# Performance work log

Measured on AMD Instinct MI355X. Metric: run time of the kernel, lower is better.

## Reference

```python
import jax, jax.numpy as jnp
import numpy as np
from jax import lax

GN_EPS = 1e-5


def _conv2d(x, w, b, pad):
    # x: (N, C, H, W), w: (O, I, kh, kw)
    y = lax.conv_general_dilated(x, w, window_strides=(1, 1),
                                 padding=[(pad, pad), (pad, pad)],
                                 dimension_numbers=('NCHW', 'OIHW', 'NCHW'))
    return y + b[None, :, None, None]


def _eca(x, eca_w, eca_b):
    # x: (N, C, H, W) -> channel attention (N, C, 1, 1)
    y = jnp.mean(x, axis=(2, 3))[:, None, :]  # (N, 1, C) : GAP then treat C as length
    y = lax.conv_general_dilated(y, eca_w, window_strides=(1,),
                                 padding=[(1, 1)],
                                 dimension_numbers=('NCH', 'OIH', 'NCH'))
    y = jax.nn.sigmoid(y + eca_b[None, :, None])  # (N, 1, C)
    return y[:, 0, :, None, None]  # (N, C, 1, 1)


def _group_norm_per_channel(x, gn_w, gn_b):
    # num_groups == num_channels: normalize each channel over (H, W)
    mean = jnp.mean(x, axis=(2, 3), keepdims=True)
    var = jnp.var(x, axis=(2, 3), keepdims=True)
    xhat = (x - mean) * lax.rsqrt(var + GN_EPS)
    return xhat * gn_w[None, :, None, None] + gn_b[None, :, None, None]


def setup_inputs() -> dict:
    key = jax.random.key(0)
    ks = jax.random.split(key, 8)
    b, c, h, w = 16, 512, 64, 64
    cg = c // 32  # 16
    s = 1.0 / np.sqrt(cg)
    return {
        'x': jax.random.normal(ks[0], (b, c, h, w), jnp.float32),
        'conv1x1_w': jax.random.normal(ks[1], (cg, cg, 1, 1), jnp.float32) * s,
        'conv1x1_b': jnp.zeros((cg,), jnp.float32),
        'conv3x3_w': jax.random.normal(ks[2], (cg, cg, 3, 3), jnp.float32) * (s / 3),
        'conv3x3_b': jnp.zeros((cg,), jnp.float32),
        'conv5x5_w': jax.random.normal(ks[3], (cg, cg, 5, 5), jnp.float32) * (s / 5),
        'conv5x5_b': jnp.zeros((cg,), jnp.float32),
        'gn_w': jnp.ones((cg,), jnp.float32),
        'gn_b': jnp.zeros((cg,), jnp.float32),
        'eca_w': jax.random.normal(ks[4], (1, 1, 3), jnp.float32) * 0.5,
        'eca_b': jnp.zeros((1,), jnp.float32),
        'groups': 32,
    }


def reference(x, conv1x1_w, conv1x1_b, conv3x3_w, conv3x3_b,
              conv5x5_w, conv5x5_b, gn_w, gn_b, eca_w, eca_b, groups):
    b, c, h, w = x.shape
    cg = c // groups
    bg = b * groups
    group_x = x.reshape(bg, cg, h, w)

    # coordinate attention branch
    x_h = jnp.mean(group_x, axis=3, keepdims=True)            # (bg, cg, h, 1)
    x_w = jnp.mean(group_x, axis=2, keepdims=True)            # (bg, cg, 1, w)
    x_w_t = jnp.transpose(x_w, (0, 1, 3, 2))                  # (bg, cg, w, 1)
    hw = _conv2d(jnp.concatenate([x_h, x_w_t], axis=2), conv1x1_w, conv1x1_b, 0)
    x_h2, x_w2 = hw[:, :, :h, :], hw[:, :, h:, :]             # (bg,cg,h,1), (bg,cg,w,1)
    gated = group_x * jax.nn.sigmoid(x_h2) * jax.nn.sigmoid(jnp.transpose(x_w2, (0, 1, 3, 2)))
    x1 = _group_norm_per_channel(gated, gn_w, gn_b)

    # parallel conv branches
    x2 = _conv2d(group_x, conv3x3_w, conv3x3_b, 1)
    x3 = _conv2d(group_x, conv5x5_w, conv5x5_b, 2)

    # shared ECA channel attention over the three branches
    ca = _eca(x1, eca_w, eca_b) + _eca(x2, eca_w, eca_b) + _eca(x3, eca_w, eca_b)
    group_x = group_x * ca

    # cross-scale softmax-bmm interactions
    def chan_softmax(v):
        # (bg, cg, h, w) -> softmax over channel means -> (bg, 1, cg)
        return jax.nn.softmax(jnp.mean(v, axis=(2, 3)), axis=-1)[:, None, :]

    x11, x21, x31 = chan_softmax(x1), chan_softmax(x2), chan_softmax(x3)
    f1 = x1.reshape(bg, cg, h * w)
    f2 = x2.reshape(bg, cg, h * w)
    f3 = x3.reshape(bg, cg, h * w)

    weights = (jnp.matmul(x11, f2) + jnp.matmul(x11, f3)
               + jnp.matmul(x21, f1) + jnp.matmul(x21, f3)
               + jnp.matmul(x31, f1) + jnp.matmul(x31, f2))  # (bg, 1, h*w)
    weights = jax.nn.sigmoid(weights.reshape(bg, 1, h, w))

    return (group_x * weights).reshape(b, c, h, w)
```

## Files before the change

kernel.cpp:

```cpp
#include <hip/hip_runtime.h>

typedef unsigned int u32;

#define CG   16
#define HWN  4096
#define LSTR 72

__device__ __forceinline__ float sigm(float x) { return 1.0f / (1.0f + __expf(-x)); }

union SharedU {
  struct {
    float row[16][64];
    float col[16][64];
    union {
      float cwave[16][4][64];
      struct { float RS[16][25]; float part2[16][16]; float part3[16][16]; } r;
    } u;
  } p;
  float cb[2][68][LSTR];
};

__global__ __launch_bounds__(256, 2) void ema_kernel(
    const float* __restrict__ x,
    const float* __restrict__ w1, const float* __restrict__ b1,
    const float* __restrict__ w3, const float* __restrict__ b3,
    const float* __restrict__ w5, const float* __restrict__ b5,
    const float* __restrict__ gnw, const float* __restrict__ gnb,
    const float* __restrict__ ew, const float* __restrict__ eb,
    float* __restrict__ out)
{
  __shared__ SharedU U;
  __shared__ float s_sh[16][64];
  __shared__ float s_sw[16][64];
  __shared__ float s_W5[16][28];
  __shared__ float s_ca[16], s_A1[16], s_Cc[16];
  __shared__ float s_w1[256], s_b1[16], s_gnw[16], s_gnb[16], s_b3[16], s_b5[16], s_ecaw[3], s_ecab[1];
  __shared__ float s_m2[16], s_m3[16], s_sm1[16], s_sm2[16], s_sm3[16];
  __shared__ float s_a1[16], s_a2[16], s_a3[16], s_total[16];
  __shared__ float s_red[16][4][2];
  __shared__ float s_scal[2];

  const int g = blockIdx.x;
  const int t = threadIdx.x;
  const float* px   = x   + (size_t)g * CG * HWN;
  float*       pout = out + (size_t)g * CG * HWN;

  {
    const int j4 = t & 15, hh = t >> 4, wv4 = t >> 6;
    for (int c = 0; c < CG; ++c) {
      float cp0 = 0.f, cp1 = 0.f, cp2 = 0.f, cp3 = 0.f;
      #pragma unroll
      for (int k = 0; k < 4; ++k) {
        int y = 4 * hh + k;
        float4 v = *(const float4*)(px + c * HWN + y * 64 + 4 * j4);
        float rs = v.x + v.y + v.z + v.w;
        rs += __shfl_xor(rs, 1); rs += __shfl_xor(rs, 2);
        rs += __shfl_xor(rs, 4); rs += __shfl_xor(rs, 8);
        if (j4 == 0) U.p.row[c][y] = rs;
        cp0 += v.x; cp1 += v.y; cp2 += v.z; cp3 += v.w;
      }
      cp0 += __shfl_xor(cp0, 16); cp0 += __shfl_xor(cp0, 32);
      cp1 += __shfl_xor(cp1, 16); cp1 += __shfl_xor(cp1, 32);
      cp2 += __shfl_xor(cp2, 16); cp2 += __shfl_xor(cp2, 32);
      cp3 += __shfl_xor(cp3, 16); cp3 += __shfl_xor(cp3, 32);
      if ((t & 48) == 0) *(float4*)&U.p.u.cwave[c][wv4][4 * j4] = make_float4(cp0, cp1, cp2, cp3);
    }
  }
  s_w1[t] = w1[t];
  if (t < 16) {
    s_b1[t]  = b1[t];  s_gnw[t] = gnw[t]; s_gnb[t] = gnb[t];
    s_b3[t]  = b3[t];  s_b5[t]  = b5[t];
  }
  if (t < 3)  s_ecaw[t] = ew[t];
  if (t == 0) s_ecab[0] = eb[0];
  __syncthreads();

  {
    int c = t >> 4, q = t & 15;
    float4 s = make_float4(0.f, 0.f, 0.f, 0.f);
    #pragma unroll
    for (int w = 0; w < 4; ++w) {
      float4 v = *(float4*)&U.p.u.cwave[c][w][4 * q];
      s.x += v.x; s.y += v.y; s.z += v.z; s.w += v.w;
    }
    *(float4*)&U.p.col[c][4 * q] = s;
  }
  __syncthreads();
  if (t < 16) { float s = 0.f; for (int y = 0; y < 64; ++y) s += U.p.row[t][y]; s_total[t] = s; }
  __syncthreads();

  for (int m = 0; m < 8; ++m) {
    int idx = t + 256 * m; int o = idx >> 7, pos = idx & 127;
    float acc = s_b1[o];
    const float inv64 = 1.0f / 64.0f;
    #pragma unroll
    for (int i = 0; i < 16; ++i) {
      float v = (pos < 64 ? U.p.row[i][pos] : U.p.col[i][pos - 64]) * inv64;
      acc += s_w1[o * 16 + i] * v;
    }
    float sg = sigm(acc);
    if (pos < 64) s_sh[o][pos] = sg; else s_sw[o][pos - 64] = sg;
  }
  for (int m = 0; m < 2; ++m) {
    int task = t + 256 * m;
    if (task < 400) {
      int i = task / 25, kk = task % 25;
      int dy = kk / 5 - 2, dx = kk % 5 - 2;
      int a  = dy > 0 ? dy : 0,   b  = 64 + (dy < 0 ? dy : 0);
      int cl = dx > 0 ? dx : 0,   d  = 64 + (dx < 0 ? dx : 0);
      float S = s_total[i];
      if (a > 0)  S -= U.p.row[i][0];
      if (a > 1)  S -= U.p.row[i][1];
      if (b < 64) S -= U.p.row[i][63];
      if (b < 63) S -= U.p.row[i][62];
      for (int x0 = 0; x0 < cl; ++x0) {
        float cv = U.p.col[i][x0];
        if (a > 0)  cv -= px[i * HWN + 0 * 64  + x0];
        if (a > 1)  cv -= px[i * HWN + 1 * 64  + x0];
        if (b < 64) cv -= px[i * HWN + 63 * 64 + x0];
        if (b < 63) cv -= px[i * HWN + 62 * 64 + x0];
        S -= cv;
      }
      for (int x0 = d; x0 < 64; ++x0) {
        float cv = U.p.col[i][x0];
        if (a > 0)  cv -= px[i * HWN + 0 * 64  + x0];
        if (a > 1)  cv -= px[i * HWN + 1 * 64  + x0];
        if (b < 64) cv -= px[i * HWN + 63 * 64 + x0];
        if (b < 63) cv -= px[i * HWN + 62 * 64 + x0];
        S -= cv;
      }
      U.p.u.r.RS[i][kk] = S;
    }
  }
  __syncthreads();

  {
    int o = t >> 4, i = t & 15;
    float p2 = 0.f, p3 = 0.f;
    const float* w3b = w3 + (o * 16 + i) * 9;
    const float* w5b = w5 + (o * 16 + i) * 25;
    #pragma unroll
    for (int ky = 0; ky < 3; ++ky)
      #pragma unroll
      for (int kx = 0; kx < 3; ++kx)
        p2 += w3b[ky * 3 + kx] * U.p.u.r.RS[i][(ky + 1) * 5 + (kx + 1)];
    #pragma unroll
    for (int kk = 0; kk < 25; ++kk) p3 += w5b[kk] * U.p.u.r.RS[i][kk];
    U.p.u.r.part2[o][i] = p2; U.p.u.r.part3[o][i] = p3;
  }
  __syncthreads();
  if (t < 16)      { float s = 0.f; for (int i = 0; i < 16; ++i) s += U.p.u.r.part2[t][i];    s_m2[t] = s_b3[t] + s * (1.0f/4096.0f); }
  else if (t < 32) { int o = t - 16; float s = 0.f; for (int i = 0; i < 16; ++i) s += U.p.u.r.part3[o][i]; s_m3[o] = s_b5[o] + s * (1.0f/4096.0f); }
  __syncthreads();

  if (t < 3) {
    const float* m = (t == 0) ? s_gnb : (t == 1) ? s_m2 : s_m3;
    float* dst     = (t == 0) ? s_sm1 : (t == 1) ? s_sm2 : s_sm3;
    float mx = m[0];
    for (int c = 1; c < 16; ++c) mx = fmaxf(mx, m[c]);
    float e[16], ssum = 0.f;
    for (int c = 0; c < 16; ++c) { e[c] = __expf(m[c] - mx); ssum += e[c]; }
    float r = 1.0f / ssum;
    for (int c = 0; c < 16; ++c) dst[c] = e[c] * r;
  }
  __syncthreads();

  if (t < 16) {
    int c = t;
    float casum = 0.f;
    #pragma unroll
    for (int v = 0; v < 3; ++v) {
      const float* m = (v == 0) ? s_gnb : (v == 1) ? s_m2 : s_m3;
      float acc = s_ecab[0] + s_ecaw[1] * m[c];
      if (c > 0)  acc += s_ecaw[0] * m[c - 1];
      if (c < 15) acc += s_ecaw[2] * m[c + 1];
      casum += sigm(acc);
    }
    s_ca[c] = casum;
    s_a1[c] = s_sm2[c] + s_sm3[c];
    s_a2[c] = s_sm1[c] + s_sm3[c];
    s_a3[c] = s_sm1[c] + s_sm2[c];
  }
  __syncthreads();

  if (t == 0) {
    float s = 0.f;
    for (int o = 0; o < 16; ++o) s += s_a2[o] * s_b3[o] + s_a3[o] * s_b5[o];
    s_scal[1] = s;
  }
  for (int m = 0; m < 2; ++m) {
    int task = t + 256 * m;
    if (task < 400) {
      int i = task / 25, kk = task % 25, ky = kk / 5, kx = kk % 5;
      float acc = 0.f;
      #pragma unroll
      for (int o = 0; o < 16; ++o) acc += s_a3[o] * w5[((o * 16 + i) * 5 + ky) * 5 + kx];
      if (ky >= 1 && ky <= 3 && kx >= 1 && kx <= 3) {
        #pragma unroll
        for (int o = 0; o < 16; ++o) acc += s_a2[o] * w3[((o * 16 + i) * 3 + (ky - 1)) * 3 + (kx - 1)];
      }
      s_W5[i][kk] = acc;
    }
    else if (task < 448) { int i = (task - 400) / 3; s_W5[i][25 + (task - 400) % 3] = 0.f; }
  }
  __syncthreads();

  for (int m = 0; m < 10; ++m) { int idx = t + 256 * m; if (idx < 2448) ((float4*)U.cb)[idx] = make_float4(0.f, 0.f, 0.f, 0.f); }
  __syncthreads();

  const int x0 = 4 * (t & 15), y0 = 4 * (t >> 4), wv4 = t >> 6;

  #define STAGE(buf, c) {                                              \
    _Pragma("unroll")                                                  \
    for (int k = 0; k < 4; ++k) {                                      \
      int q = t + 256 * k;                                             \
      int rr = q >> 4, xc = (q & 15) * 4;                              \
      float4 v = *(const float4*)(px + (c) * HWN + rr * 64 + xc);      \
      float* d = &U.cb[buf][2 + rr][2 + xc];                           \
      *(float2*)d       = make_float2(v.x, v.y);                       \
      *(float2*)(d + 2) = make_float2(v.z, v.w);                       \
    }                                                                  \
  }

  float ws[16];
  #pragma unroll
  for (int i = 0; i < 16; ++i) ws[i] = 0.f;

  STAGE(0, 0);
  __syncthreads();
  #pragma unroll 1
  for (int c = 0; c < 16; ++c) {
    if (c < 15) STAGE((c + 1) & 1, c + 1);
    float Wk[28];
    #pragma unroll
    for (int i = 0; i < 7; ++i) *(float4*)&Wk[4 * i] = *(float4*)&s_W5[c][4 * i];
    float shv[4], swv[4];
    #pragma unroll
    for (int r = 0; r < 4; ++r) { shv[r] = s_sh[c][y0 + r]; swv[r] = s_sw[c][x0 + r]; }
    const float* base = &U.cb[c & 1][0][0];
    float gsl = 0.f, gql = 0.f;
    #pragma unroll
    for (int q = 0; q < 8; ++q) {
      const float* rp = base + (y0 + q) * LSTR + x0;
      float4 A = *(const float4*)rp, B = *(const float4*)(rp + 4);
      float v[8] = {A.x, A.y, A.z, A.w, B.x, B.y, B.z, B.w};
      if (q >= 2 && q <= 5) {
        const int ry = q - 2;
        #pragma unroll
        for (int m = 0; m < 4; ++m) { float gg = v[m + 2] * shv[ry] * swv[m]; gsl += gg; gql += gg * gg; }
      }
      #pragma unroll
      for (int r = 0; r < 4; ++r) {
        if (q - r >= 0 && q - r <= 4) {
          const int kr = q - r;
          #pragma unroll
          for (int m = 0; m < 4; ++m) {
            float a = ws[4 * r + m];
            a += Wk[kr * 5 + 0] * v[m + 0];
            a += Wk[kr * 5 + 1] * v[m + 1];
            a += Wk[kr * 5 + 2] * v[m + 2];
            a += Wk[kr * 5 + 3] * v[m + 3];
            a += Wk[kr * 5 + 4] * v[m + 4];
            ws[4 * r + m] = a;
          }
        }
      }
    }
    gsl += __shfl_xor(gsl, 1);  gql += __shfl_xor(gql, 1);
    gsl += __shfl_xor(gsl, 2);  gql += __shfl_xor(gql, 2);
    gsl += __shfl_xor(gsl, 4);  gql += __shfl_xor(gql, 4);
    gsl += __shfl_xor(gsl, 8);  gql += __shfl_xor(gql, 8);
    gsl += __shfl_xor(gsl, 16); gql += __shfl_xor(gql, 16);
    gsl += __shfl_xor(gsl, 32); gql += __shfl_xor(gql, 32);
    if ((t & 63) == 0) { s_red[c][wv4][0] = gsl; s_red[c][wv4][1] = gql; }
    __syncthreads();
  }

  if (t < 16) {
    int c = t;
    float S = 0.f, Q = 0.f;
    #pragma unroll
    for (int w = 0; w < 4; ++w) { S += s_red[c][w][0]; Q += s_red[c][w][1]; }
    float mu  = S * (1.0f / 4096.0f);
    float var = Q * (1.0f / 4096.0f) - mu * mu;
    float inv = rsqrtf(var + 1e-5f);
    s_A1[c] = s_a1[c] * s_gnw[c] * inv;
    s_Cc[c] = s_a1[c] * (s_gnb[c] - mu * s_gnw[c] * inv);
  }
  __syncthreads();
  if (t == 0) { float s = s_scal[1]; for (int c = 0; c < 16; ++c) s += s_Cc[c]; s_scal[0] = s; }
  for (int m = 0; m < 4; ++m) { int idx = t + 256 * m; int c = idx >> 6, y = idx & 63; s_sh[c][y] *= s_A1[c]; }
  __syncthreads();

  float gws[16];
  #pragma unroll
  for (int i = 0; i < 16; ++i) gws[i] = 0.f;
  #pragma unroll 1
  for (int c = 0; c < 16; ++c) {
    float shv[4], swv[4];
    #pragma unroll
    for (int r = 0; r < 4; ++r) { shv[r] = s_sh[c][y0 + r]; swv[r] = s_sw[c][x0 + r]; }
    #pragma unroll
    for (int r = 0; r < 4; ++r) {
      float4 xv = *(const float4*)(px + c * HWN + (y0 + r) * 64 + x0);
      gws[4 * r + 0] += shv[r] * swv[0] * xv.x;
      gws[4 * r + 1] += shv[r] * swv[1] * xv.y;
      gws[4 * r + 2] += shv[r] * swv[2] * xv.z;
      gws[4 * r + 3] += shv[r] * swv[3] * xv.w;
    }
  }
  {
    const float Cc = s_scal[0];
    #pragma unroll
    for (int i = 0; i < 16; ++i) ws[i] = sigm(ws[i] + gws[i] + Cc);
  }
  #pragma unroll 1
  for (int c = 0; c < 16; ++c) {
    float cav = s_ca[c];
    #pragma unroll
    for (int r = 0; r < 4; ++r) {
      float4 xv = *(const float4*)(px + c * HWN + (y0 + r) * 64 + x0);
      float4 o;
      o.x = xv.x * cav * ws[4 * r + 0];
      o.y = xv.y * cav * ws[4 * r + 1];
      o.z = xv.z * cav * ws[4 * r + 2];
      o.w = xv.w * cav * ws[4 * r + 3];
      *(float4*)(pout + c * HWN + (y0 + r) * 64 + x0) = o;
    }
  }
}

extern "C" void kernel_launch(void* const* d_in, const int* in_sizes, int n_in,
                              void* d_out, int out_size, void* d_ws, size_t ws_size,
                              hipStream_t stream) {
  const float* X  = (const float*)d_in[0];
  const float* W1 = (const float*)d_in[1];
  const float* B1 = (const float*)d_in[2];
  const float* W3 = (const float*)d_in[3];
  const float* B3 = (const float*)d_in[4];
  const float* W5 = (const float*)d_in[5];
  const float* B5 = (const float*)d_in[6];
  const float* GW = (const float*)d_in[7];
  const float* GB = (const float*)d_in[8];
  const float* EW = (const float*)d_in[9];
  const float* EB = (const float*)d_in[10];
  float* O = (float*)d_out;
  ema_kernel<<<dim3(512), dim3(256), 0, stream>>>(X, W1, B1, W3, B3, W5, B5, GW, GB, EW, EB, O);
}
```

Before: 345.5 us.

## Double block size, fuse GN-gate pass into conv loop with deferred per-channel scaling

Launches 512 threads per group block, so each thread handles a 2x4 output tile instead of 4x4. The first-pass reductions are restructured so each wave owns two channels, which removes the cross-wave column reduction and one barrier. The separate pass that re-read x for the gated GroupNorm contribution is removed. Instead, gated values are kept in registers and folded into the accumulator with a two-channel lag once each channel's GN statistics are ready. The shared-memory union is dropped in favour of separate arrays with a tighter LDS stride, which raises LDS use and register pressure in exchange for fewer global re-reads and barriers.

```diff
diff --git a/kernel.cpp b/kernel.cpp
--- a/kernel.cpp
+++ b/kernel.cpp
@@ -4,23 +4,11 @@
 
 #define CG   16
 #define HWN  4096
-#define LSTR 72
+#define LSTR 68
 
 __device__ __forceinline__ float sigm(float x) { return 1.0f / (1.0f + __expf(-x)); }
 
-union SharedU {
-  struct {
-    float row[16][64];
-    float col[16][64];
-    union {
-      float cwave[16][4][64];
-      struct { float RS[16][25]; float part2[16][16]; float part3[16][16]; } r;
-    } u;
-  } p;
-  float cb[2][68][LSTR];
-};
-
-__global__ __launch_bounds__(256, 2) void ema_kernel(
+__global__ __launch_bounds__(512, 4) void ema_kernel(
     const float* __restrict__ x,
     const float* __restrict__ w1, const float* __restrict__ b1,
     const float* __restrict__ w3, const float* __restrict__ b3,
@@ -29,44 +17,57 @@
     const float* __restrict__ ew, const float* __restrict__ eb,
     float* __restrict__ out)
 {
-  __shared__ SharedU U;
-  __shared__ float s_sh[16][64];
-  __shared__ float s_sw[16][64];
-  __shared__ float s_W5[16][28];
+  __shared__ __align__(16) float s_cb[2][68][LSTR];
+  __shared__ __align__(16) float s_row[16][64];
+  __shared__ __align__(16) float s_col[16][64];
+  __shared__ __align__(16) float s_RS[16][25];
+  __shared__ float s_p2[16][16], s_p3[16][16];
+  __shared__ __align__(16) float s_sh[16][64];
+  __shared__ __align__(16) float s_sw[16][64];
+  __shared__ __align__(16) float s_W5[16][28];
   __shared__ float s_ca[16], s_A1[16], s_Cc[16];
   __shared__ float s_w1[256], s_b1[16], s_gnw[16], s_gnb[16], s_b3[16], s_b5[16], s_ecaw[3], s_ecab[1];
   __shared__ float s_m2[16], s_m3[16], s_sm1[16], s_sm2[16], s_sm3[16];
   __shared__ float s_a1[16], s_a2[16], s_a3[16], s_total[16];
-  __shared__ float s_red[16][4][2];
+  __shared__ float s_red[16][8][2];
   __shared__ float s_scal[2];
 
   const int g = blockIdx.x;
   const int t = threadIdx.x;
+  const int wv = t >> 6;
+  const int ln = t & 63;
   const float* px   = x   + (size_t)g * CG * HWN;
   float*       pout = out + (size_t)g * CG * HWN;
 
   {
-    const int j4 = t & 15, hh = t >> 4, wv4 = t >> 6;
-    for (int c = 0; c < CG; ++c) {
+    const int j4 = ln & 15;
+    const int rr = ln >> 4;
+    #pragma unroll 1
+    for (int cc = 0; cc < 2; ++cc) {
+      const int c = 2 * wv + cc;
+      float rs[16];
       float cp0 = 0.f, cp1 = 0.f, cp2 = 0.f, cp3 = 0.f;
       #pragma unroll
-      for (int k = 0; k < 4; ++k) {
-        int y = 4 * hh + k;
-        float4 v = *(const float4*)(px + c * HWN + y * 64 + 4 * j4);
-        float rs = v.x + v.y + v.z + v.w;
-        rs += __shfl_xor(rs, 1); rs += __shfl_xor(rs, 2);
-        rs += __shfl_xor(rs, 4); rs += __shfl_xor(rs, 8);
-        if (j4 == 0) U.p.row[c][y] = rs;
+      for (int j = 0; j < 16; ++j) {
+        float4 v = *(const float4*)(px + c * HWN + (rr + 4 * j) * 64 + 4 * j4);
+        rs[j] = v.x + v.y + v.z + v.w;
         cp0 += v.x; cp1 += v.y; cp2 += v.z; cp3 += v.w;
+      }
+      #pragma unroll
+      for (int j = 0; j < 16; ++j) {
+        float r = rs[j];
+        r += __shfl_xor(r, 1); r += __shfl_xor(r, 2);
+        r += __shfl_xor(r, 4); r += __shfl_xor(r, 8);
+        if (j4 == 0) s_row[c][rr + 4 * j] = r;
       }
       cp0 += __shfl_xor(cp0, 16); cp0 += __shfl_xor(cp0, 32);
       cp1 += __shfl_xor(cp1, 16); cp1 += __shfl_xor(cp1, 32);
       cp2 += __shfl_xor(cp2, 16); cp2 += __shfl_xor(cp2, 32);
       cp3 += __shfl_xor(cp3, 16); cp3 += __shfl_xor(cp3, 32);
-      if ((t & 48) == 0) *(float4*)&U.p.u.cwave[c][wv4][4 * j4] = make_float4(cp0, cp1, cp2, cp3);
-    }
-  }
-  s_w1[t] = w1[t];
+      if (rr == 0) *(float4*)&s_col[c][4 * j4] = make_float4(cp0, cp1, cp2, cp3);
+    }
+  }
+  if (t < 256) s_w1[t] = w1[t];
   if (t < 16) {
     s_b1[t]  = b1[t];  s_gnw[t] = gnw[t]; s_gnb[t] = gnb[t];
     s_b3[t]  = b3[t];  s_b5[t]  = b5[t];
@@ -75,66 +76,55 @@
   if (t == 0) s_ecab[0] = eb[0];
   __syncthreads();
 
-  {
-    int c = t >> 4, q = t & 15;
-    float4 s = make_float4(0.f, 0.f, 0.f, 0.f);
-    #pragma unroll
-    for (int w = 0; w < 4; ++w) {
-      float4 v = *(float4*)&U.p.u.cwave[c][w][4 * q];
-      s.x += v.x; s.y += v.y; s.z += v.z; s.w += v.w;
-    }
-    *(float4*)&U.p.col[c][4 * q] = s;
-  }
-  __syncthreads();
-  if (t < 16) { float s = 0.f; for (int y = 0; y < 64; ++y) s += U.p.row[t][y]; s_total[t] = s; }
-  __syncthreads();
-
-  for (int m = 0; m < 8; ++m) {
-    int idx = t + 256 * m; int o = idx >> 7, pos = idx & 127;
+  if (t < 16) { float s = 0.f; for (int y = 0; y < 64; ++y) s += s_row[t][y]; s_total[t] = s; }
+  __syncthreads();
+
+  #pragma unroll
+  for (int m = 0; m < 4; ++m) {
+    int idx = t + 512 * m; int o = idx >> 7, pos = idx & 127;
     float acc = s_b1[o];
     const float inv64 = 1.0f / 64.0f;
     #pragma unroll
     for (int i = 0; i < 16; ++i) {
-      float v = (pos < 64 ? U.p.row[i][pos] : U.p.col[i][pos - 64]) * inv64;
+      float v = (pos < 64 ? s_row[i][pos] : s_col[i][pos - 64]) * inv64;
       acc += s_w1[o * 16 + i] * v;
     }
     float sg = sigm(acc);
     if (pos < 64) s_sh[o][pos] = sg; else s_sw[o][pos - 64] = sg;
   }
-  for (int m = 0; m < 2; ++m) {
-    int task = t + 256 * m;
-    if (task < 400) {
-      int i = task / 25, kk = task % 25;
-      int dy = kk / 5 - 2, dx = kk % 5 - 2;
-      int a  = dy > 0 ? dy : 0,   b  = 64 + (dy < 0 ? dy : 0);
-      int cl = dx > 0 ? dx : 0,   d  = 64 + (dx < 0 ? dx : 0);
-      float S = s_total[i];
-      if (a > 0)  S -= U.p.row[i][0];
-      if (a > 1)  S -= U.p.row[i][1];
-      if (b < 64) S -= U.p.row[i][63];
-      if (b < 63) S -= U.p.row[i][62];
-      for (int x0 = 0; x0 < cl; ++x0) {
-        float cv = U.p.col[i][x0];
-        if (a > 0)  cv -= px[i * HWN + 0 * 64  + x0];
-        if (a > 1)  cv -= px[i * HWN + 1 * 64  + x0];
-        if (b < 64) cv -= px[i * HWN + 63 * 64 + x0];
-        if (b < 63) cv -= px[i * HWN + 62 * 64 + x0];
-        S -= cv;
-      }
-      for (int x0 = d; x0 < 64; ++x0) {
-        float cv = U.p.col[i][x0];
-        if (a > 0)  cv -= px[i * HWN + 0 * 64  + x0];
-        if (a > 1)  cv -= px[i * HWN + 1 * 64  + x0];
-        if (b < 64) cv -= px[i * HWN + 63 * 64 + x0];
-        if (b < 63) cv -= px[i * HWN + 62 * 64 + x0];
-        S -= cv;
-      }
-      U.p.u.r.RS[i][kk] = S;
-    }
-  }
-  __syncthreads();
-
-  {
+  #pragma unroll
+  for (int m = 0; m < 5; ++m) { int idx = t + 512 * m; if (idx < 2312) ((float4*)s_cb)[idx] = make_float4(0.f, 0.f, 0.f, 0.f); }
+  if (t < 400) {
+    int i = t / 25, kk = t % 25;
+    int dy = kk / 5 - 2, dx = kk % 5 - 2;
+    int a  = dy > 0 ? dy : 0,   b  = 64 + (dy < 0 ? dy : 0);
+    int cl = dx > 0 ? dx : 0,   d  = 64 + (dx < 0 ? dx : 0);
+    float S = s_total[i];
+    if (a > 0)  S -= s_row[i][0];
+    if (a > 1)  S -= s_row[i][1];
+    if (b < 64) S -= s_row[i][63];
+    if (b < 63) S -= s_row[i][62];
+    for (int x0 = 0; x0 < cl; ++x0) {
+      float cv = s_col[i][x0];
+      if (a > 0)  cv -= px[i * HWN + 0 * 64  + x0];
+      if (a > 1)  cv -= px[i * HWN + 1 * 64  + x0];
+      if (b < 64) cv -= px[i * HWN + 63 * 64 + x0];
+      if (b < 63) cv -= px[i * HWN + 62 * 64 + x0];
+      S -= cv;
+    }
+    for (int x0 = d; x0 < 64; ++x0) {
+      float cv = s_col[i][x0];
+      if (a > 0)  cv -= px[i * HWN + 0 * 64  + x0];
+      if (a > 1)  cv -= px[i * HWN + 1 * 64  + x0];
+      if (b < 64) cv -= px[i * HWN + 63 * 64 + x0];
+      if (b < 63) cv -= px[i * HWN + 62 * 64 + x0];
+      S -= cv;
+    }
+    s_RS[i][kk] = S;
+  }
+  __syncthreads();
+
+  if (t < 256) {
     int o = t >> 4, i = t & 15;
     float p2 = 0.f, p3 = 0.f;
     const float* w3b = w3 + (o * 16 + i) * 9;
@@ -143,14 +133,14 @@
     for (int ky = 0; ky < 3; ++ky)
       #pragma unroll
       for (int kx = 0; kx < 3; ++kx)
-        p2 += w3b[ky * 3 + kx] * U.p.u.r.RS[i][(ky + 1) * 5 + (kx + 1)];
-    #pragma unroll
-    for (int kk = 0; kk < 25; ++kk) p3 += w5b[kk] * U.p.u.r.RS[i][kk];
-    U.p.u.r.part2[o][i] = p2; U.p.u.r.part3[o][i] = p3;
-  }
-  __syncthreads();
-  if (t < 16)      { float s = 0.f; for (int i = 0; i < 16; ++i) s += U.p.u.r.part2[t][i];    s_m2[t] = s_b3[t] + s * (1.0f/4096.0f); }
-  else if (t < 32) { int o = t - 16; float s = 0.f; for (int i = 0; i < 16; ++i) s += U.p.u.r.part3[o][i]; s_m3[o] = s_b5[o] + s * (1.0f/4096.0f); }
+        p2 += w3b[ky * 3 + kx] * s_RS[i][(ky + 1) * 5 + (kx + 1)];
+    #pragma unroll
+    for (int kk = 0; kk < 25; ++kk) p3 += w5b[kk] * s_RS[i][kk];
+    s_p2[o][i] = p2; s_p3[o][i] = p3;
+  }
+  __syncthreads();
+  if (t < 16)      { float s = 0.f; for (int i = 0; i < 16; ++i) s += s_p2[t][i];      s_m2[t] = s_b3[t] + s * (1.0f/4096.0f); }
+  else if (t < 32) { int o = t - 16; float s = 0.f; for (int i = 0; i < 16; ++i) s += s_p3[o][i]; s_m3[o] = s_b5[o] + s * (1.0f/4096.0f); }
   __syncthreads();
 
   if (t < 3) {
@@ -183,15 +173,26 @@
   }
   __syncthreads();
 
+  #define STAGE(buf, c) {                                                \
+    _Pragma("unroll")                                                    \
+    for (int k = 0; k < 2; ++k) {                                        \
+      int q = t + 512 * k;                                               \
+      int rr = q >> 4, xc = (q & 15) * 4;                                \
+      float4 v = *(const float4*)(px + (size_t)(c) * HWN + rr * 64 + xc);\
+      float* d = &s_cb[buf][2 + rr][2 + xc];                             \
+      *(float2*)d       = make_float2(v.x, v.y);                         \
+      *(float2*)(d + 2) = make_float2(v.z, v.w);                         \
+    }                                                                    \
+  }
+
   if (t == 0) {
     float s = 0.f;
     for (int o = 0; o < 16; ++o) s += s_a2[o] * s_b3[o] + s_a3[o] * s_b5[o];
     s_scal[1] = s;
   }
-  for (int m = 0; m < 2; ++m) {
-    int task = t + 256 * m;
-    if (task < 400) {
-      int i = task / 25, kk = task % 25, ky = kk / 5, kx = kk % 5;
+  if (t < 448) {
+    if (t < 400) {
+      int i = t / 25, kk = t % 25, ky = kk / 5, kx = kk % 5;
       float acc = 0.f;
       #pragma unroll
       for (int o = 0; o < 16; ++o) acc += s_a3[o] * w5[((o * 16 + i) * 5 + ky) * 5 + kx];
@@ -200,59 +201,67 @@
         for (int o = 0; o < 16; ++o) acc += s_a2[o] * w3[((o * 16 + i) * 3 + (ky - 1)) * 3 + (kx - 1)];
       }
       s_W5[i][kk] = acc;
-    }
-    else if (task < 448) { int i = (task - 400) / 3; s_W5[i][25 + (task - 400) % 3] = 0.f; }
-  }
-  __syncthreads();
-
-  for (int m = 0; m < 10; ++m) { int idx = t + 256 * m; if (idx < 2448) ((float4*)U.cb)[idx] = make_float4(0.f, 0.f, 0.f, 0.f); }
-  __syncthreads();
-
-  const int x0 = 4 * (t & 15), y0 = 4 * (t >> 4), wv4 = t >> 6;
-
-  #define STAGE(buf, c) {                                              \
-    _Pragma("unroll")                                                  \
-    for (int k = 0; k < 4; ++k) {                                      \
-      int q = t + 256 * k;                                             \
-      int rr = q >> 4, xc = (q & 15) * 4;                              \
-      float4 v = *(const float4*)(px + (c) * HWN + rr * 64 + xc);      \
-      float* d = &U.cb[buf][2 + rr][2 + xc];                           \
-      *(float2*)d       = make_float2(v.x, v.y);                       \
-      *(float2*)(d + 2) = make_float2(v.z, v.w);                       \
-    }                                                                  \
-  }
-
-  float ws[16];
+    } else {
+      int q = t - 400; s_W5[q / 3][25 + q % 3] = 0.f;
+    }
+  }
+  STAGE(0, 0);
+  __syncthreads();
+
+  const int x0 = 4 * (t & 15);
+  const int y0 = 2 * (t >> 4);
+
+  float ws[8];
   #pragma unroll
-  for (int i = 0; i < 16; ++i) ws[i] = 0.f;
-
-  STAGE(0, 0);
-  __syncthreads();
+  for (int i = 0; i < 8; ++i) ws[i] = 0.f;
+  float gsv[2][8];
+
   #pragma unroll 1
   for (int c = 0; c < 16; ++c) {
     if (c < 15) STAGE((c + 1) & 1, c + 1);
+    if (c >= 1 && t == 0) {
+      float S = 0.f, Q = 0.f;
+      #pragma unroll
+      for (int w = 0; w < 8; ++w) { S += s_red[c-1][w][0]; Q += s_red[c-1][w][1]; }
+      float mu  = S * (1.0f / 4096.0f);
+      float var = Q * (1.0f / 4096.0f) - mu * mu;
+      float inv = rsqrtf(var + 1e-5f);
+      s_A1[c-1] = s_a1[c-1] * s_gnw[c-1] * inv;
+      s_Cc[c-1] = s_a1[c-1] * (s_gnb[c-1] - mu * s_gnw[c-1] * inv);
+    }
+    if (c >= 2) {
+      float a1v = s_A1[c-2];
+      #pragma unroll
+      for (int i = 0; i < 8; ++i) ws[i] += a1v * gsv[c & 1][i];
+    }
     float Wk[28];
     #pragma unroll
     for (int i = 0; i < 7; ++i) *(float4*)&Wk[4 * i] = *(float4*)&s_W5[c][4 * i];
-    float shv[4], swv[4];
-    #pragma unroll
-    for (int r = 0; r < 4; ++r) { shv[r] = s_sh[c][y0 + r]; swv[r] = s_sw[c][x0 + r]; }
-    const float* base = &U.cb[c & 1][0][0];
+    float shv0 = s_sh[c][y0], shv1 = s_sh[c][y0 + 1];
+    float swv[4];
+    #pragma unroll
+    for (int r = 0; r < 4; ++r) swv[r] = s_sw[c][x0 + r];
+    const float* base = &s_cb[c & 1][0][0] + y0 * LSTR + x0;
     float gsl = 0.f, gql = 0.f;
     #pragma unroll
-    for (int q = 0; q < 8; ++q) {
-      const float* rp = base + (y0 + q) * LSTR + x0;
+    for (int q = 0; q < 6; ++q) {
+      const float* rp = base + q * LSTR;
       float4 A = *(const float4*)rp, B = *(const float4*)(rp + 4);
       float v[8] = {A.x, A.y, A.z, A.w, B.x, B.y, B.z, B.w};
-      if (q >= 2 && q <= 5) {
-        const int ry = q - 2;
+      if (q == 2 || q == 3) {
+        const float sh_ = (q == 2) ? shv0 : shv1;
+        const int ri = q - 2;
         #pragma unroll
-        for (int m = 0; m < 4; ++m) { float gg = v[m + 2] * shv[ry] * swv[m]; gsl += gg; gql += gg * gg; }
-      }
-      #pragma unroll
-      for (int r = 0; r < 4; ++r) {
-        if (q - r >= 0 && q - r <= 4) {
-          const int kr = q - r;
+        for (int m = 0; m < 4; ++m) {
+          float gg = v[m + 2] * sh_ * swv[m];
+          gsl += gg; gql += gg * gg;
+          gsv[c & 1][4 * ri + m] = gg;
+        }
+      }
+      #pragma unroll
+      for (int r = 0; r < 2; ++r) {
+        const int kr = q - r;
+        if (kr >= 0 && kr <= 4) {
           #pragma unroll
           for (int m = 0; m < 4; ++m) {
             float a = ws[4 * r + m];
@@ -272,61 +281,45 @@
     gsl += __shfl_xor(gsl, 8);  gql += __shfl_xor(gql, 8);
     gsl += __shfl_xor(gsl, 16); gql += __shfl_xor(gql, 16);
     gsl += __shfl_xor(gsl, 32); gql += __shfl_xor(gql, 32);
-    if ((t & 63) == 0) { s_red[c][wv4][0] = gsl; s_red[c][wv4][1] = gql; }
+    if (ln == 0) { s_red[c][wv][0] = gsl; s_red[c][wv][1] = gql; }
     __syncthreads();
   }
 
-  if (t < 16) {
-    int c = t;
+  if (t == 0) {
     float S = 0.f, Q = 0.f;
     #pragma unroll
-    for (int w = 0; w < 4; ++w) { S += s_red[c][w][0]; Q += s_red[c][w][1]; }
+    for (int w = 0; w < 8; ++w) { S += s_red[15][w][0]; Q += s_red[15][w][1]; }
     float mu  = S * (1.0f / 4096.0f);
     float var = Q * (1.0f / 4096.0f) - mu * mu;
     float inv = rsqrtf(var + 1e-5f);
-    s_A1[c] = s_a1[c] * s_gnw[c] * inv;
-    s_Cc[c] = s_a1[c] * (s_gnb[c] - mu * s_gnw[c] * inv);
-  }
-  __syncthreads();
-  if (t == 0) { float s = s_scal[1]; for (int c = 0; c < 16; ++c) s += s_Cc[c]; s_scal[0] = s; }
-  for (int m = 0; m < 4; ++m) { int idx = t + 256 * m; int c = idx >> 6, y = idx & 63; s_sh[c][y] *= s_A1[c]; }
-  __syncthreads();
-
-  float gws[16];
+    s_A1[15] = s_a1[15] * s_gnw[15] * inv;
+    s_Cc[15] = s_a1[15] * (s_gnb[15] - mu * s_gnw[15] * inv);
+    float s = s_scal[1];
+    for (int c = 0; c < 16; ++c) s += s_Cc[c];
+    s_scal[0] = s;
+  }
+  __syncthreads();
+  {
+    const float a14 = s_A1[14], a15 = s_A1[15], Ct = s_scal[0];
+    #pragma unroll
+    for (int i = 0; i < 8; ++i)
+      ws[i] = sigm(ws[i] + a14 * gsv[0][i] + a15 * gsv[1][i] + Ct);
+  }
+
   #pragma unroll
-  for (int i = 0; i < 16; ++i) gws[i] = 0.f;
-  #pragma unroll 1
   for (int c = 0; c < 16; ++c) {
-    float shv[4], swv[4];
-    #pragma unroll
-    for (int r = 0; r < 4; ++r) { shv[r] = s_sh[c][y0 + r]; swv[r] = s_sw[c][x0 + r]; }
-    #pragma unroll
-    for (int r = 0; r < 4; ++r) {
-      float4 xv = *(const float4*)(px + c * HWN + (y0 + r) * 64 + x0);
-      gws[4 * r + 0] += shv[r] * swv[0] * xv.x;
-      gws[4 * r + 1] += shv[r] * swv[1] * xv.y;
-      gws[4 * r + 2] += shv[r] * swv[2] * xv.z;
-      gws[4 * r + 3] += shv[r] * swv[3] * xv.w;
-    }
-  }
-  {
-    const float Cc = s_scal[0];
-    #pragma unroll
-    for (int i = 0; i < 16; ++i) ws[i] = sigm(ws[i] + gws[i] + Cc);
-  }
-  #pragma unroll 1
-  for (int c = 0; c < 16; ++c) {
-    float cav = s_ca[c];
-    #pragma unroll
-    for (int r = 0; r < 4; ++r) {
-      float4 xv = *(const float4*)(px + c * HWN + (y0 + r) * 64 + x0);
-      float4 o;
-      o.x = xv.x * cav * ws[4 * r + 0];
-      o.y = xv.y * cav * ws[4 * r + 1];
-      o.z = xv.z * cav * ws[4 * r + 2];
-      o.w = xv.w * cav * ws[4 * r + 3];
-      *(float4*)(pout + c * HWN + (y0 + r) * 64 + x0) = o;
-    }
+    const float cav = s_ca[c];
+    const float* xp = px   + c * HWN + y0 * 64 + x0;
+    float*       op = pout + c * HWN + y0 * 64 + x0;
+    float4 xa = *(const float4*)xp;
+    float4 xb = *(const float4*)(xp + 64);
+    float4 oa, ob;
+    oa.x = xa.x * cav * ws[0]; oa.y = xa.y * cav * ws[1];
+    oa.z = xa.z * cav * ws[2]; oa.w = xa.w * cav * ws[3];
+    ob.x = xb.x * cav * ws[4]; ob.y = xb.y * cav * ws[5];
+    ob.z = xb.z * cav * ws[6]; ob.w = xb.w * cav * ws[7];
+    *(float4*)op        = oa;
+    *(float4*)(op + 64) = ob;
   }
 }
 
@@ -345,5 +338,5 @@
   const float* EW = (const float*)d_in[9];
   const float* EB = (const float*)d_in[10];
   float* O = (float*)d_out;
-  ema_kernel<<<dim3(512), dim3(256), 0, stream>>>(X, W1, B1, W3, B3, W5, B5, GW, GB, EW, EB, O);
+  ema_kernel<<<dim3(512), dim3(512), 0, stream>>>(X, W1, B1, W3, B3, W5, B5, GW, GB, EW, EB, O);
 }
```

Result: no change. 345.3 us (-0.1%).
